# Optimization experiments

Hardware: AMD Instinct MI355X
Metric: run time of the kernel (lower is better)

Reference implementation:

```python
import jax, jax.numpy as jnp
import numpy as np

# Device / mapping constants (from iterator config in the original repo)
V_REF = 0.25
K_V = 2.0 * V_REF
G_MIN = 1e-5
G_MAX = 1e-3
N_AVG = 2.99
N_STD = 0.37
N_IN, N_OUT, BATCH = 1024, 512, 128


def setup_inputs() -> dict:
    key = jax.random.key(0)
    ks = jax.random.split(key, 6)
    x = jax.random.uniform(ks[0], (BATCH, N_IN), dtype=jnp.float32)
    stdv = 1.0 / np.sqrt(N_IN)
    w_pos = 0.5 + stdv * jax.random.normal(ks[1], (N_IN, N_OUT), dtype=jnp.float32)
    w_neg = 0.5 + stdv * jax.random.normal(ks[2], (N_IN, N_OUT), dtype=jnp.float32)
    b_pos = 0.5 * jnp.ones((N_OUT,), jnp.float32)
    b_neg = 0.5 * jnp.ones((N_OUT,), jnp.float32)
    # per-crosspoint I-V nonlinearity parameter n (n=2 means ohmic); clip below at 2
    n_devices = jnp.maximum(
        N_AVG + N_STD * jax.random.normal(ks[3], (N_IN + 1, 2 * N_OUT), dtype=jnp.float32),
        2.0,
    )
    return {"x": x, "w_pos": w_pos, "w_neg": w_neg, "b_pos": b_pos,
            "b_neg": b_neg, "n_devices": n_devices}


def reference(x, w_pos, w_neg, b_pos, b_neg, n_devices):
    B = x.shape[0]
    # append bias input of 1s -> [B, n_in+1]
    inputs = jnp.concatenate([x, jnp.ones((B, 1), x.dtype)], axis=1)
    # combined weights with bias row -> [n_in+1, n_out] each
    cw_pos = jnp.concatenate([w_pos, b_pos[None, :]], axis=0)
    cw_neg = jnp.concatenate([w_neg, b_neg[None, :]], axis=0)
    # interleave pos/neg columns -> [n_in+1, 2*n_out]
    combined = jnp.stack([cw_pos, cw_neg], axis=-1).reshape(cw_pos.shape[0], -1)
    # x -> V mapping
    V = K_V * inputs  # [B, n_in+1]
    # weight params -> conductances
    max_weight = jnp.max(jnp.abs(combined))
    k_G = (G_MAX - G_MIN) / max_weight
    G = k_G * jnp.abs(combined) + G_MIN  # [n_in+1, 2*n_out]
    # nonlinear I-V: I(V) = sign(V) * G*V_ref * (|V|/V_ref)^log2(n)
    exponent = jnp.log2(n_devices)          # [n_in+1, 2*n_out]
    sgn = jnp.sign(V)                       # [B, n_in+1]
    ratio = jnp.abs(V) / V_REF              # [B, n_in+1]
    I_ind = (sgn[:, :, None] * (G * V_REF)[None, :, :]
             * ratio[:, :, None] ** exponent[None, :, :])  # [B, n_in+1, 2*n_out]
    I = jnp.sum(I_ind, axis=1)              # [B, 2*n_out] (sum along bit lines)
    # differential pair currents -> output
    I_total = I[:, 0::2] - I[:, 1::2]       # [B, n_out]
    y = I_total / (K_V * k_G)
    return y
```

## Files before the change

### kernel.cpp

```cpp
#include <hip/hip_runtime.h>
#include <cstdint>
#include <cstddef>


#define B128 128
#define NIN  1024
#define NI   1025
#define NO   512
#define NJ   1024
#define GMIN 1.0e-5f
#define GSPAN (1.0e-3f - 1.0e-5f)
#define ZCH  8
#define CHUNK 128

__device__ __forceinline__ float flog2(float x) { return __builtin_amdgcn_logf(x); }
__device__ __forceinline__ float fexp2(float x) { return __builtin_amdgcn_exp2f(x); }

__global__ __launch_bounds__(1024) void k_prep(
    const float* __restrict__ x,
    const float* __restrict__ wp, const float* __restrict__ wn,
    const float* __restrict__ bp, const float* __restrict__ bn,
    float* __restrict__ LT, float* __restrict__ bmax, float* __restrict__ out)
{
    const int tid = blockIdx.x * 1024 + threadIdx.x;

    if (tid < B128 * NO) out[tid] = 0.0f;

    if (tid < NI * B128) {
        int i = tid >> 7, b = tid & 127;
        float xv = (i < NIN) ? x[b * NIN + i] : 1.0f;
        LT[tid] = 1.0f + flog2(xv);
    }

    float m = fmaxf(fmaxf(__builtin_fabsf(wp[tid]), __builtin_fabsf(wn[tid])),
                    fmaxf(__builtin_fabsf(wp[tid + 262144]), __builtin_fabsf(wn[tid + 262144])));
    if (tid < NO) m = fmaxf(m, fmaxf(__builtin_fabsf(bp[tid]), __builtin_fabsf(bn[tid])));

    __shared__ float red[16];
    #pragma unroll
    for (int off = 32; off > 0; off >>= 1) m = fmaxf(m, __shfl_down(m, off, 64));
    if ((threadIdx.x & 63) == 0) red[threadIdx.x >> 6] = m;
    __syncthreads();
    if (threadIdx.x < 16) {
        m = red[threadIdx.x];
        #pragma unroll
        for (int off = 8; off > 0; off >>= 1) m = fmaxf(m, __shfl_down(m, off, 16));
        if (threadIdx.x == 0) bmax[blockIdx.x] = m;
    }
}

__global__ __launch_bounds__(512) void k_tab(
    const float* __restrict__ nd,
    const float* __restrict__ wp, const float* __restrict__ wn,
    const float* __restrict__ bp, const float* __restrict__ bn,
    const float* __restrict__ bmax,
    float4* __restrict__ ew, float* __restrict__ biasv)
{
    const int i = blockIdx.x;
    const int o = threadIdx.x;
    const int lane = threadIdx.x & 63;

    float m = fmaxf(fmaxf(bmax[lane], bmax[lane + 64]),
                    fmaxf(bmax[lane + 128], bmax[lane + 192]));
    #pragma unroll
    for (int off = 32; off > 0; off >>= 1) m = fmaxf(m, __shfl_down(m, off, 64));
    const float maxw = __shfl(m, 0, 64);
    const float hdelta = 0.5f * (maxw * (GMIN / GSPAN));

    const float2 nv = *(const float2*)(nd + (size_t)i * NJ + 2 * o);
    if (i < NIN) {
        const float wvp = __builtin_fabsf(wp[(size_t)i * NO + o]);
        const float wvn = __builtin_fabsf(wn[(size_t)i * NO + o]);
        ew[(size_t)i * NO + o] = make_float4(
            flog2(nv.x), flog2(nv.y),
            flog2(__builtin_fmaf(0.5f, wvp, hdelta)),
            flog2(__builtin_fmaf(0.5f, wvn, hdelta)));
    } else {
        const float gp = __builtin_fmaf(0.5f, __builtin_fabsf(bp[o]), hdelta);
        const float gn = __builtin_fmaf(0.5f, __builtin_fabsf(bn[o]), hdelta);
        biasv[o] = nv.x * gp - nv.y * gn;
    }
}

__global__ __launch_bounds__(512) void k_main(
    const float4* __restrict__ ew, const float* __restrict__ LT,
    const float* __restrict__ biasv, float* __restrict__ out)
{
    const int lane = threadIdx.x & 63;
    const int s    = threadIdx.x >> 6;
    const int o    = (blockIdx.x << 6) + lane;
    const int b0   = blockIdx.y << 4;
    const int i0   = blockIdx.z * CHUNK + s;

    const float4* pEW = ew + (size_t)i0 * NO + o;
    const float*  pL  = LT + (size_t)i0 * B128 + b0;

    float accp[16], accn[16];
    #pragma unroll
    for (int k = 0; k < 16; ++k) { accp[k] = 0.0f; accn[k] = 0.0f; }

    float4 e0 = pEW[0];
    float4 e1 = pEW[8 * NO];
    const float4* pE = pEW + 16 * NO;
    float4 La = *(const float4*)(pL);
    float4 Lb = *(const float4*)(pL + 4);
    float4 Lc = *(const float4*)(pL + 8);
    float4 Ld = *(const float4*)(pL + 12);

#define STEP(E) do { \
        const float Lv[16] = {La.x, La.y, La.z, La.w, Lb.x, Lb.y, Lb.z, Lb.w, \
                              Lc.x, Lc.y, Lc.z, Lc.w, Ld.x, Ld.y, Ld.z, Ld.w}; \
        _Pragma("unroll") \
        for (int j = 0; j < 16; ++j) { \
            accp[j] += fexp2(__builtin_fmaf((E).x, Lv[j], (E).z)); \
            accn[j] += fexp2(__builtin_fmaf((E).y, Lv[j], (E).w)); \
        } \
    } while (0)

    #pragma unroll 2
    for (int k = 0; k < 14; ++k) {
        const float4 e2 = *pE;
        pE += 8 * NO;
        pL += 8 * B128;
        const float4 Lan = *(const float4*)(pL);
        const float4 Lbn = *(const float4*)(pL + 4);
        const float4 Lcn = *(const float4*)(pL + 8);
        const float4 Ldn = *(const float4*)(pL + 12);

        STEP(e0);

        e0 = e1; e1 = e2;
        La = Lan; Lb = Lbn; Lc = Lcn; Ld = Ldn;
    }
    {
        pL += 8 * B128;
        const float4 Lan = *(const float4*)(pL);
        const float4 Lbn = *(const float4*)(pL + 4);
        const float4 Lcn = *(const float4*)(pL + 8);
        const float4 Ldn = *(const float4*)(pL + 12);
        STEP(e0);
        e0 = e1;
        La = Lan; Lb = Lbn; Lc = Lcn; Ld = Ldn;
    }
    STEP(e0);
#undef STEP

    __shared__ float lds[8 * 64 * 33];
    {
        const int base = (s * 64 + lane) * 33;
        #pragma unroll
        for (int j = 0; j < 16; ++j) { lds[base + j] = accp[j]; lds[base + 16 + j] = accn[j]; }
    }
    __syncthreads();

    float bias = 0.0f;
    if (blockIdx.z == 0) bias = biasv[o];

    {
        const int l = threadIdx.x & 63;
        #pragma unroll
        for (int r = 0; r < 2; ++r) {
            const int bb = (threadIdx.x >> 6) + (r << 3);
            float sum = bias;
            #pragma unroll
            for (int w = 0; w < 8; ++w) {
                const int base = (w * 64 + l) * 33;
                sum += lds[base + bb] - lds[base + 16 + bb];
            }
            unsafeAtomicAdd(out + (size_t)(b0 + bb) * NO + (blockIdx.x << 6) + l, sum);
        }
    }
}

extern "C" void kernel_launch(void* const* d_in, const int* in_sizes, int n_in,
                              void* d_out, int out_size, void* d_ws, size_t ws_size,
                              hipStream_t stream)
{
    const float* x  = (const float*)d_in[0];
    const float* wp = (const float*)d_in[1];
    const float* wn = (const float*)d_in[2];
    const float* bp = (const float*)d_in[3];
    const float* bn = (const float*)d_in[4];
    const float* nd = (const float*)d_in[5];
    float* out = (float*)d_out;

    unsigned char* ws = (unsigned char*)d_ws;
    float*  bmax  = (float*)ws;
    float*  LT    = (float*)(ws + 4096);
    float4* EW    = (float4*)(ws + 528896);
    float*  biasv = (float*)(ws + 8917504);

    k_prep<<<256, 1024, 0, stream>>>(x, wp, wn, bp, bn, LT, bmax, out);
    k_tab<<<NI, 512, 0, stream>>>(nd, wp, wn, bp, bn, bmax, EW, biasv);
    k_main<<<dim3(8, 8, ZCH), 512, 0, stream>>>(EW, LT, biasv, out);
}
```

Baseline: 92.35 us.

## Halve per-thread batch tile in main kernel to raise occupancy

Each thread in k_main now accumulates 8 batch rows instead of 16, and the grid's batch dimension doubles to 16 blocks. This cuts register use and LDS footprint, and launch bounds request 8 waves per EU. The pos/neg difference is taken before the LDS write, so the cross-wave reduction reads half as much shared memory. The wave index is made scalar with readfirstlane. In exchange, each ew float4 is loaded by twice as many blocks, roughly doubling global/L2 traffic for the table, and twice as many blocks do atomic adds into the output.

```diff
diff --git a/kernel.cpp b/kernel.cpp
--- a/kernel.cpp
+++ b/kernel.cpp
@@ -82,36 +82,33 @@
     }
 }
 
-__global__ __launch_bounds__(512) void k_main(
+__global__ __launch_bounds__(512, 8) void k_main(
     const float4* __restrict__ ew, const float* __restrict__ LT,
     const float* __restrict__ biasv, float* __restrict__ out)
 {
     const int lane = threadIdx.x & 63;
-    const int s    = threadIdx.x >> 6;
+    const int sw   = __builtin_amdgcn_readfirstlane(threadIdx.x >> 6);
     const int o    = (blockIdx.x << 6) + lane;
-    const int b0   = blockIdx.y << 4;
-    const int i0   = blockIdx.z * CHUNK + s;
+    const int b0   = blockIdx.y << 3;
+    const int i0   = blockIdx.z * CHUNK + sw;
 
-    const float4* pEW = ew + (size_t)i0 * NO + o;
-    const float*  pL  = LT + (size_t)i0 * B128 + b0;
+    const float4* pE = ew + (size_t)i0 * NO + o;
+    const float*  pL = LT + i0 * B128 + b0;
 
-    float accp[16], accn[16];
+    float accp[8], accn[8];
     #pragma unroll
-    for (int k = 0; k < 16; ++k) { accp[k] = 0.0f; accn[k] = 0.0f; }
+    for (int j = 0; j < 8; ++j) { accp[j] = 0.0f; accn[j] = 0.0f; }
 
-    float4 e0 = pEW[0];
-    float4 e1 = pEW[8 * NO];
-    const float4* pE = pEW + 16 * NO;
+    float4 e0 = pE[0];
+    float4 e1 = pE[8 * NO];
+    pE += 16 * NO;
     float4 La = *(const float4*)(pL);
     float4 Lb = *(const float4*)(pL + 4);
-    float4 Lc = *(const float4*)(pL + 8);
-    float4 Ld = *(const float4*)(pL + 12);
 
 #define STEP(E) do { \
-        const float Lv[16] = {La.x, La.y, La.z, La.w, Lb.x, Lb.y, Lb.z, Lb.w, \
-                              Lc.x, Lc.y, Lc.z, Lc.w, Ld.x, Ld.y, Ld.z, Ld.w}; \
+        const float Lv[8] = {La.x, La.y, La.z, La.w, Lb.x, Lb.y, Lb.z, Lb.w}; \
         _Pragma("unroll") \
-        for (int j = 0; j < 16; ++j) { \
+        for (int j = 0; j < 8; ++j) { \
             accp[j] += fexp2(__builtin_fmaf((E).x, Lv[j], (E).z)); \
             accn[j] += fexp2(__builtin_fmaf((E).y, Lv[j], (E).w)); \
         } \
@@ -124,52 +121,36 @@
         pL += 8 * B128;
         const float4 Lan = *(const float4*)(pL);
         const float4 Lbn = *(const float4*)(pL + 4);
-        const float4 Lcn = *(const float4*)(pL + 8);
-        const float4 Ldn = *(const float4*)(pL + 12);
 
         STEP(e0);
 
         e0 = e1; e1 = e2;
-        La = Lan; Lb = Lbn; Lc = Lcn; Ld = Ldn;
+        La = Lan; Lb = Lbn;
     }
     {
         pL += 8 * B128;
         const float4 Lan = *(const float4*)(pL);
         const float4 Lbn = *(const float4*)(pL + 4);
-        const float4 Lcn = *(const float4*)(pL + 8);
-        const float4 Ldn = *(const float4*)(pL + 12);
         STEP(e0);
         e0 = e1;
-        La = Lan; Lb = Lbn; Lc = Lcn; Ld = Ldn;
+        La = Lan; Lb = Lbn;
     }
     STEP(e0);
 #undef STEP
 
-    __shared__ float lds[8 * 64 * 33];
+    __shared__ float lds[8 * 64 * 9];
     {
-        const int base = (s * 64 + lane) * 33;
+        const int base = (sw * 64 + lane) * 9;
         #pragma unroll
-        for (int j = 0; j < 16; ++j) { lds[base + j] = accp[j]; lds[base + 16 + j] = accn[j]; }
+        for (int j = 0; j < 8; ++j) lds[base + j] = accp[j] - accn[j];
     }
     __syncthreads();
 
-    float bias = 0.0f;
-    if (blockIdx.z == 0) bias = biasv[o];
-
-    {
-        const int l = threadIdx.x & 63;
-        #pragma unroll
-        for (int r = 0; r < 2; ++r) {
-            const int bb = (threadIdx.x >> 6) + (r << 3);
-            float sum = bias;
-            #pragma unroll
-            for (int w = 0; w < 8; ++w) {
-                const int base = (w * 64 + l) * 33;
-                sum += lds[base + bb] - lds[base + 16 + bb];
-            }
-            unsafeAtomicAdd(out + (size_t)(b0 + bb) * NO + (blockIdx.x << 6) + l, sum);
-        }
-    }
+    float sum = 0.0f;
+    #pragma unroll
+    for (int w = 0; w < 8; ++w) sum += lds[(w * 64 + lane) * 9 + sw];
+    if (blockIdx.z == 0) sum += biasv[o];
+    unsafeAtomicAdd(out + (size_t)(b0 + sw) * NO + o, sum);
 }
 
 extern "C" void kernel_launch(void* const* d_in, const int* in_sizes, int n_in,
@@ -192,5 +173,5 @@
 
     k_prep<<<256, 1024, 0, stream>>>(x, wp, wn, bp, bn, LT, bmax, out);
     k_tab<<<NI, 512, 0, stream>>>(nd, wp, wn, bp, bn, bmax, EW, biasv);
-    k_main<<<dim3(8, 8, ZCH), 512, 0, stream>>>(EW, LT, biasv, out);
+    k_main<<<dim3(8, 16, ZCH), 512, 0, stream>>>(EW, LT, biasv, out);
 }
```

Result: no change. 93.33 us (+1.1%).
